# Performance work log

Hardware: AMD Instinct MI355X
Metric: run time of the kernel (lower is better)

## Reference

```python
import jax, jax.numpy as jnp
import numpy as np

B, N, F_IN, F_OUT, H = 8, 1024, 64, 128, 4
D = F_OUT // H  # head_dim = 32
NEG_SLOPE = 0.2


def setup_inputs() -> dict:
    key = jax.random.key(0)
    k1, k2, k3, k4, k5 = jax.random.split(key, 5)
    x = jax.random.normal(k1, (B, N, F_IN), dtype=jnp.float32)
    adj = jax.random.randint(k2, (N, N), 0, 2, dtype=jnp.int32)
    edge_weights = jax.random.uniform(k3, (N, N), dtype=jnp.float32)
    W = jax.random.normal(k4, (F_IN, F_OUT), dtype=jnp.float32) * (1.0 / np.sqrt(F_IN))
    a = jax.random.normal(k5, (H, 2 * D), dtype=jnp.float32) * (1.0 / np.sqrt(2 * D))
    return {"x": x, "adj": adj, "edge_weights": edge_weights, "W": W, "a": a}


def reference(x, adj, edge_weights, W, a):
    # x: [B,N,F_in], adj: [N,N] int, edge_weights: [N,N], W: [F_in,F_out], a: [H,2D]
    b, n, _ = x.shape
    h = (x @ W).reshape(b, n, H, D)  # [B,N,H,D]
    # e[b,i,j,h] = leaky_relu(a_src . h_i + a_dst . h_j)  (equivalent to concat trick)
    e_src = jnp.einsum('bnhd,hd->bnh', h, a[:, :D])  # [B,N,H]
    e_dst = jnp.einsum('bnhd,hd->bnh', h, a[:, D:])  # [B,N,H]
    e = jax.nn.leaky_relu(e_src[:, :, None, :] + e_dst[:, None, :, :], NEG_SLOPE)  # [B,N,N,H]
    mask = (adj == 0)[None, :, :, None]  # [1,N,N,1]
    e = jnp.where(mask, -jnp.inf, e)
    # numerically-stable softmax over neighbors (axis=2), matching torch reference
    e_max = jnp.max(e, axis=2, keepdims=True)
    e_max = jnp.where(jnp.isinf(e_max), 0.0, e_max)
    e_stable = e - e_max
    e_stable = jnp.where(jnp.isinf(e_stable), -100.0, e_stable)
    attn = jax.nn.softmax(e_stable, axis=2)
    attn = jnp.where(jnp.isnan(attn), 0.0, attn)
    # dropout is identity in eval mode
    attn = attn * edge_weights[None, :, :, None]  # [B,N,N,H]
    out = jnp.einsum('bijh,bjhd->bihd', attn, h).reshape(b, n, H * D)  # [B,N,F_out]
    avg_attn = attn.mean(axis=-1)  # [B,N,N]
    return out, avg_attn
```

## Files before the change

### kernel.cpp

```cpp
#include <hip/hip_runtime.h>
#include <hip/hip_bf16.h>

constexpr int B  = 8;
constexpr int N  = 1024;
constexpr int FI = 64;
constexpr int FO = 128;
constexpr int NH = 4;
constexpr float LOG2E = 1.4426950408889634f;

using short8 = __attribute__((ext_vector_type(8))) short;
using f32x4  = __attribute__((ext_vector_type(4))) float;

union I8 { int4 v[2]; int s[8]; };
union F8 { float4 v[2]; float s[8]; };

__device__ __forceinline__ unsigned bfpack(float a, float b) {
  __hip_bfloat162 r = __float22bfloat162_rn(make_float2(a, b));
  union { __hip_bfloat162 h; unsigned u; } c; c.h = r; return c.u;
}
__device__ __forceinline__ float bf2f(unsigned short u) {
  union { unsigned int b; float f; } c; c.b = (unsigned int)u << 16; return c.f;
}

__global__ __launch_bounds__(256) void gat_mask(
    const int* __restrict__ adj, const float* __restrict__ ew,
    unsigned short* __restrict__ mew) {
  const size_t base = ((size_t)blockIdx.x * 256 + threadIdx.x) * 8;
  I8 aj; aj.v[0] = *(const int4*)(adj + base); aj.v[1] = *(const int4*)(adj + base + 4);
  F8 e;  e.v[0]  = *(const float4*)(ew + base); e.v[1]  = *(const float4*)(ew + base + 4);
  union { unsigned short u[8]; uint4 v; } o;
  #pragma unroll
  for (int u = 0; u < 8; ++u) {
    __hip_bfloat16 hb = __float2bfloat16(e.s[u]);
    unsigned short bits = *reinterpret_cast<unsigned short*>(&hb);
    o.u[u] = aj.s[u] ? bits : (unsigned short)0x8000;
  }
  *(uint4*)(mew + base) = o.v;
}

__global__ __launch_bounds__(256, 2) void gat_proj(
    const float* __restrict__ x, const float* __restrict__ W,
    const float* __restrict__ a,
    unsigned short* __restrict__ h_hi, unsigned short* __restrict__ h_lo,
    float* __restrict__ es, float* __restrict__ edt) {
  __shared__ float xs[16 * FI];
  const int t = threadIdx.x;
  const int row0 = blockIdx.x * 16;
  for (int i = t; i < 16 * FI; i += 256) xs[i] = x[row0 * FI + i];
  const int f  = t & 127;
  const int rh = t >> 7;
  float wc[FI];
  #pragma unroll
  for (int k = 0; k < FI; ++k) wc[k] = W[k * FO + f];
  const int hh = f >> 5, d = f & 31;
  const float a_s = a[hh * 64 + d] * LOG2E;
  const float a_d = a[hh * 64 + 32 + d] * LOG2E;
  __syncthreads();
  float acc8[8];
  #pragma unroll
  for (int r = 0; r < 8; ++r) {
    const int lr = rh * 8 + r;
    const float4* xr = (const float4*)(xs + lr * FI);
    float acc = 0.f;
    #pragma unroll
    for (int kq = 0; kq < FI / 4; ++kq) {
      const float4 xv = xr[kq];
      acc += xv.x * wc[4*kq] + xv.y * wc[4*kq+1] + xv.z * wc[4*kq+2] + xv.w * wc[4*kq+3];
    }
    acc8[r] = acc;
    float ps = acc * a_s, pd = acc * a_d;
    #pragma unroll
    for (int off = 16; off; off >>= 1) {
      ps += __shfl_xor(ps, off, 64);
      pd += __shfl_xor(pd, off, 64);
    }
    const int row = row0 + lr;
    if (d == 0) {
      es[row * NH + hh] = ps;
      edt[((size_t)((row >> 10) * NH + hh)) * N + (row & 1023)] = pd;
    }
  }
  const int bb = row0 >> 10;
  const int jl = (row0 & 1023) + rh * 8;
  union { unsigned short u16[8]; uint4 v; } hi, lo;
  #pragma unroll
  for (int r = 0; r < 8; ++r) {
    __hip_bfloat16 hb = __float2bfloat16(acc8[r]);
    hi.u16[r] = *reinterpret_cast<unsigned short*>(&hb);
    float res = acc8[r] - __bfloat162float(hb);
    __hip_bfloat16 lb = __float2bfloat16(res);
    lo.u16[r] = *reinterpret_cast<unsigned short*>(&lb);
  }
  const int ft = f >> 4, n = f & 15;
  const int sS = jl >> 5, kq2 = (jl >> 3) & 3;
  const size_t base = (size_t)bb * (FO * N)
                    + ((size_t)(ft * 32 + sS) * 64 + (n + 16 * kq2)) * 8;
  *(uint4*)(h_hi + base) = hi.v;
  *(uint4*)(h_lo + base) = lo.v;
}

__global__ __launch_bounds__(512, 2) void gat_attn(
    const unsigned short* __restrict__ h_hi, const unsigned short* __restrict__ h_lo,
    const float* __restrict__ es, const float* __restrict__ edt,
    const unsigned short* __restrict__ mew,
    float* __restrict__ out, float* __restrict__ dinv) {
  __shared__ unsigned short pew[2][4 * 2048];
  __shared__ float dvl[64];
  const int t  = threadIdx.x;
  const int b  = blockIdx.x & 7;
  const int i0 = (blockIdx.x >> 3) << 4;
  const int il = t >> 5, jq = t & 31;
  const int gi = i0 + il;
  float esv[4];
  { const float4 e4 = *(const float4*)(es + ((size_t)b * N + gi) * NH);
    esv[0] = e4.x; esv[1] = e4.y; esv[2] = e4.z; esv[3] = e4.w; }
  const int lane = t & 63, wave = t >> 6;
  const int hh = wave & 3, nt2 = wave >> 2;
  const int m = lane & 15, kq = lane >> 4;
  const int ft = hh * 2 + nt2;
  const unsigned short* hb_hi = h_hi + (size_t)b * (FO * N) + (size_t)(ft * 32) * 512 + lane * 8;
  const unsigned short* hb_lo = h_lo + (size_t)b * (FO * N) + (size_t)(ft * 32) * 512 + lane * 8;
  f32x4 acc0 = {0.f,0.f,0.f,0.f}, acc1 = {0.f,0.f,0.f,0.f};
  f32x4 acc2 = {0.f,0.f,0.f,0.f}, acc3 = {0.f,0.f,0.f,0.f};
  float dpart[4] = {0.f, 0.f, 0.f, 0.f};

  auto p1_step = [&](int c, int buf) {
    const int jb = c * 128 + jq * 4;
    union { unsigned v2[2]; unsigned short u[4]; } mw;
    *(uint2*)mw.v2 = *(const uint2*)(mew + (size_t)gi * N + jb);
    float edh[4][4];
    #pragma unroll
    for (int h = 0; h < 4; ++h) {
      const float4 e4 = *(const float4*)(edt + ((size_t)(b * NH + h)) * N + jb);
      edh[h][0] = e4.x; edh[h][1] = e4.y; edh[h][2] = e4.z; edh[h][3] = e4.w;
    }
    float pw[4][4];
    #pragma unroll
    for (int u = 0; u < 4; ++u) {
      const float mfa = bf2f((unsigned short)(mw.u[u] & 0x7fff));
      const float sgn = (mw.u[u] >> 15) ? 0.f : 1.f;
      #pragma unroll
      for (int h = 0; h < 4; ++h) {
        float e = esv[h] + edh[h][u];
        e = fmaxf(e, 0.2f * e);
        const float p = __builtin_amdgcn_exp2f(e);
        pw[h][u] = p * mfa;
        dpart[h] = fmaf(p, sgn, dpart[h]);
      }
    }
    const int g = jq >> 1, half = jq & 1;
    const int o = ((g * 16 + il) ^ (g & 7)) * 8 + half * 4;
    #pragma unroll
    for (int h = 0; h < 4; ++h) {
      uint2 pk = { bfpack(pw[h][0], pw[h][1]), bfpack(pw[h][2], pw[h][3]) };
      *(uint2*)(pew[buf] + h * 2048 + o) = pk;
    }
  };

  short8 Bh[4], Bl[4];
  #pragma unroll
  for (int ks = 0; ks < 4; ++ks) {
    Bh[ks] = *(const short8*)(hb_hi + (size_t)ks * 512);
    Bl[ks] = *(const short8*)(hb_lo + (size_t)ks * 512);
  }
  p1_step(0, 0);
  __syncthreads();

  for (int c = 0; c < 8; ++c) {
    short8 Ph[4], Pl[4];
    if (c + 1 < 8) {
      p1_step(c + 1, (c + 1) & 1);
      const size_t so = (size_t)(c + 1) * 4 * 512;
      #pragma unroll
      for (int ks = 0; ks < 4; ++ks) {
        Ph[ks] = *(const short8*)(hb_hi + so + (size_t)ks * 512);
        Pl[ks] = *(const short8*)(hb_lo + so + (size_t)ks * 512);
      }
    }
    {
      const int buf = c & 1;
      #pragma unroll
      for (int ks = 0; ks < 4; ++ks) {
        const int g2 = ks * 4 + kq;
        const int o2 = ((g2 * 16 + m) ^ (g2 & 7)) * 8;
        short8 afr;
        { uint4 tmp = *(const uint4*)(pew[buf] + hh * 2048 + o2);
          __builtin_memcpy(&afr, &tmp, 16); }
        if (ks & 1) {
          acc2 = __builtin_amdgcn_mfma_f32_16x16x32_bf16(afr, Bh[ks], acc2, 0, 0, 0);
          acc3 = __builtin_amdgcn_mfma_f32_16x16x32_bf16(afr, Bl[ks], acc3, 0, 0, 0);
        } else {
          acc0 = __builtin_amdgcn_mfma_f32_16x16x32_bf16(afr, Bh[ks], acc0, 0, 0, 0);
          acc1 = __builtin_amdgcn_mfma_f32_16x16x32_bf16(afr, Bl[ks], acc1, 0, 0, 0);
        }
      }
    }
    if (c + 1 < 8) __syncthreads();
    #pragma unroll
    for (int ks = 0; ks < 4; ++ks) { Bh[ks] = Ph[ks]; Bl[ks] = Pl[ks]; }
  }

  #pragma unroll
  for (int h = 0; h < 4; ++h) {
    float v = dpart[h];
    v += __shfl_xor(v, 1, 64);  v += __shfl_xor(v, 2, 64);
    v += __shfl_xor(v, 4, 64);  v += __shfl_xor(v, 8, 64);
    v += __shfl_xor(v, 16, 64);
    if (jq == 0) dvl[il * NH + h] = v;
  }
  __syncthreads();
  if (t < 64) { const float dd = dvl[t]; dvl[t] = dd > 0.f ? 1.0f / dd : 0.f; }
  __syncthreads();
  if (t < 64) dinv[((size_t)b * N + i0) * NH + t] = dvl[t];
  #pragma unroll
  for (int reg = 0; reg < 4; ++reg) {
    const int row = kq * 4 + reg;
    const float inv = dvl[row * NH + hh];
    out[((size_t)b * N + i0 + row) * FO + hh * 32 + nt2 * 16 + m]
        = (acc0[reg] + acc1[reg] + acc2[reg] + acc3[reg]) * inv;
  }
}

__global__ __launch_bounds__(256, 4) void gat_avg(
    const float* __restrict__ es, const float* __restrict__ edt,
    const unsigned short* __restrict__ mew, const float* __restrict__ dinv,
    float* __restrict__ avg) {
  const int t  = threadIdx.x;
  const int b  = blockIdx.x & 7;
  const int i0 = (blockIdx.x >> 3) << 2;
  const int il = t >> 6, jq = t & 63;
  const int gi = i0 + il;
  float esv[4], inv4[4];
  { const float4 e4 = *(const float4*)(es + ((size_t)b * N + gi) * NH);
    esv[0] = e4.x; esv[1] = e4.y; esv[2] = e4.z; esv[3] = e4.w; }
  { const float4 d4 = *(const float4*)(dinv + ((size_t)b * N + gi) * NH);
    inv4[0] = d4.x; inv4[1] = d4.y; inv4[2] = d4.z; inv4[3] = d4.w; }
  #pragma unroll
  for (int c = 0; c < 4; ++c) {
    const int jb = c * 256 + jq * 4;
    union { uint2 v; unsigned short u[4]; } mw;
    mw.v = *(const uint2*)(mew + (size_t)gi * N + jb);
    float edh[4][4];
    #pragma unroll
    for (int h = 0; h < 4; ++h) {
      const float4 e4 = *(const float4*)(edt + ((size_t)(b * NH + h)) * N + jb);
      edh[h][0] = e4.x; edh[h][1] = e4.y; edh[h][2] = e4.z; edh[h][3] = e4.w;
    }
    float4 r;
    float* rp = &r.x;
    #pragma unroll
    for (int u = 0; u < 4; ++u) {
      const float mfa = bf2f((unsigned short)(mw.u[u] & 0x7fff));
      float sv = 0.f;
      #pragma unroll
      for (int h = 0; h < 4; ++h) {
        float e = esv[h] + edh[h][u];
        e = fmaxf(e, 0.2f * e);
        sv += __builtin_amdgcn_exp2f(e) * inv4[h];
      }
      rp[u] = 0.25f * mfa * sv;
    }
    *(float4*)(avg + ((size_t)b * N + gi) * N + jb) = r;
  }
}

extern "C" void kernel_launch(void* const* d_in, const int* in_sizes, int n_in,
                              void* d_out, int out_size, void* d_ws, size_t ws_size,
                              hipStream_t stream) {
  const float* x   = (const float*)d_in[0];
  const int*   adj = (const int*)d_in[1];
  const float* ewt = (const float*)d_in[2];
  const float* W   = (const float*)d_in[3];
  const float* a   = (const float*)d_in[4];

  float* out = (float*)d_out;
  float* avg = out + (size_t)B * N * FO;

  unsigned short* hhi = (unsigned short*)d_ws;
  unsigned short* hlo = hhi + (size_t)B * FO * N;
  unsigned short* mew = hlo + (size_t)B * FO * N;
  float* es   = (float*)(mew + (size_t)N * N);
  float* edt  = es + (size_t)B * N * NH;
  float* dnv  = edt + (size_t)B * NH * N;

  gat_mask<<<(N * N) / 2048, 256, 0, stream>>>(adj, ewt, mew);
  gat_proj<<<(B * N) / 16, 256, 0, stream>>>(x, W, a, hhi, hlo, es, edt);
  gat_attn<<<B * (N / 16), 512, 0, stream>>>(hhi, hlo, es, edt, mew, out, dnv);
  gat_avg<<<B * (N / 4), 256, 0, stream>>>(es, edt, mew, dnv, avg);
}
```

Baseline: 115.4 us.

## Fuse mask/proj kernels and fold avg-attention pass into attention kernel

The mask-building and projection kernels are merged into one launch, with blocks split by index. The separate avg-attention kernel is removed: each attention block writes its own avg_attn rows right after computing the softmax denominators, so the dinv round trip and two launches go away. The main loop is also restructured to issue next-chunk loads earlier. Occupancy is raised to 4 blocks per CU, which may add register pressure or spills.

Result: faster. 110.0 us (-4.7%).

```diff
diff --git a/kernel.cpp b/kernel.cpp
--- a/kernel.cpp
+++ b/kernel.cpp
@@ -22,29 +22,29 @@
   union { unsigned int b; float f; } c; c.b = (unsigned int)u << 16; return c.f;
 }
 
-__global__ __launch_bounds__(256) void gat_mask(
-    const int* __restrict__ adj, const float* __restrict__ ew,
+__global__ __launch_bounds__(256, 2) void gat_prep(
+    const float* __restrict__ x, const float* __restrict__ W,
+    const float* __restrict__ a, const int* __restrict__ adj,
+    const float* __restrict__ ew,
+    unsigned short* __restrict__ h_hi, unsigned short* __restrict__ h_lo,
+    float* __restrict__ es, float* __restrict__ edt,
     unsigned short* __restrict__ mew) {
-  const size_t base = ((size_t)blockIdx.x * 256 + threadIdx.x) * 8;
-  I8 aj; aj.v[0] = *(const int4*)(adj + base); aj.v[1] = *(const int4*)(adj + base + 4);
-  F8 e;  e.v[0]  = *(const float4*)(ew + base); e.v[1]  = *(const float4*)(ew + base + 4);
-  union { unsigned short u[8]; uint4 v; } o;
-  #pragma unroll
-  for (int u = 0; u < 8; ++u) {
-    __hip_bfloat16 hb = __float2bfloat16(e.s[u]);
-    unsigned short bits = *reinterpret_cast<unsigned short*>(&hb);
-    o.u[u] = aj.s[u] ? bits : (unsigned short)0x8000;
-  }
-  *(uint4*)(mew + base) = o.v;
-}
-
-__global__ __launch_bounds__(256, 2) void gat_proj(
-    const float* __restrict__ x, const float* __restrict__ W,
-    const float* __restrict__ a,
-    unsigned short* __restrict__ h_hi, unsigned short* __restrict__ h_lo,
-    float* __restrict__ es, float* __restrict__ edt) {
+  const int t = threadIdx.x;
+  if (blockIdx.x >= 512) {
+    const size_t base = ((size_t)(blockIdx.x - 512) * 256 + t) * 8;
+    I8 aj; aj.v[0] = *(const int4*)(adj + base); aj.v[1] = *(const int4*)(adj + base + 4);
+    F8 e;  e.v[0]  = *(const float4*)(ew + base); e.v[1]  = *(const float4*)(ew + base + 4);
+    union { unsigned short u[8]; uint4 v; } o;
+    #pragma unroll
+    for (int u = 0; u < 8; ++u) {
+      __hip_bfloat16 hb = __float2bfloat16(e.s[u]);
+      unsigned short bits = *reinterpret_cast<unsigned short*>(&hb);
+      o.u[u] = aj.s[u] ? bits : (unsigned short)0x8000;
+    }
+    *(uint4*)(mew + base) = o.v;
+    return;
+  }
   __shared__ float xs[16 * FI];
-  const int t = threadIdx.x;
   const int row0 = blockIdx.x * 16;
   for (int i = t; i < 16 * FI; i += 256) xs[i] = x[row0 * FI + i];
   const int f  = t & 127;
@@ -99,11 +99,11 @@
   *(uint4*)(h_lo + base) = lo.v;
 }
 
-__global__ __launch_bounds__(512, 2) void gat_attn(
+__global__ __launch_bounds__(512, 4) void gat_attn(
     const unsigned short* __restrict__ h_hi, const unsigned short* __restrict__ h_lo,
     const float* __restrict__ es, const float* __restrict__ edt,
     const unsigned short* __restrict__ mew,
-    float* __restrict__ out, float* __restrict__ dinv) {
+    float* __restrict__ out, float* __restrict__ avg) {
   __shared__ unsigned short pew[2][4 * 2048];
   __shared__ float dvl[64];
   const int t  = threadIdx.x;
@@ -124,80 +124,88 @@
   f32x4 acc2 = {0.f,0.f,0.f,0.f}, acc3 = {0.f,0.f,0.f,0.f};
   float dpart[4] = {0.f, 0.f, 0.f, 0.f};
 
-  auto p1_step = [&](int c, int buf) {
+  uint2  rmw;
+  float4 red[4];
+  short8 Bh[4], Bl[4];
+
+  auto ld_p1 = [&](int c) {
     const int jb = c * 128 + jq * 4;
-    union { unsigned v2[2]; unsigned short u[4]; } mw;
-    *(uint2*)mw.v2 = *(const uint2*)(mew + (size_t)gi * N + jb);
-    float edh[4][4];
-    #pragma unroll
-    for (int h = 0; h < 4; ++h) {
-      const float4 e4 = *(const float4*)(edt + ((size_t)(b * NH + h)) * N + jb);
-      edh[h][0] = e4.x; edh[h][1] = e4.y; edh[h][2] = e4.z; edh[h][3] = e4.w;
-    }
-    float pw[4][4];
-    #pragma unroll
-    for (int u = 0; u < 4; ++u) {
-      const float mfa = bf2f((unsigned short)(mw.u[u] & 0x7fff));
-      const float sgn = (mw.u[u] >> 15) ? 0.f : 1.f;
-      #pragma unroll
-      for (int h = 0; h < 4; ++h) {
-        float e = esv[h] + edh[h][u];
-        e = fmaxf(e, 0.2f * e);
-        const float p = __builtin_amdgcn_exp2f(e);
-        pw[h][u] = p * mfa;
-        dpart[h] = fmaf(p, sgn, dpart[h]);
-      }
-    }
+    rmw = *(const uint2*)(mew + (size_t)gi * N + jb);
+    #pragma unroll
+    for (int h = 0; h < 4; ++h)
+      red[h] = *(const float4*)(edt + ((size_t)(b * NH + h)) * N + jb);
+  };
+  auto ld_B = [&](int c) {
+    const size_t so = (size_t)c * 4 * 512;
+    #pragma unroll
+    for (int ks = 0; ks < 4; ++ks) {
+      Bh[ks] = *(const short8*)(hb_hi + so + (size_t)ks * 512);
+      Bl[ks] = *(const short8*)(hb_lo + so + (size_t)ks * 512);
+    }
+  };
+  auto p1_compute = [&](int c) {
+    const int buf = c & 1;
+    union { uint2 v; unsigned short u[4]; } mw; mw.v = rmw;
     const int g = jq >> 1, half = jq & 1;
     const int o = ((g * 16 + il) ^ (g & 7)) * 8 + half * 4;
     #pragma unroll
-    for (int h = 0; h < 4; ++h) {
-      uint2 pk = { bfpack(pw[h][0], pw[h][1]), bfpack(pw[h][2], pw[h][3]) };
-      *(uint2*)(pew[buf] + h * 2048 + o) = pk;
-    }
-  };
-
-  short8 Bh[4], Bl[4];
-  #pragma unroll
-  for (int ks = 0; ks < 4; ++ks) {
-    Bh[ks] = *(const short8*)(hb_hi + (size_t)ks * 512);
-    Bl[ks] = *(const short8*)(hb_lo + (size_t)ks * 512);
-  }
-  p1_step(0, 0);
-  __syncthreads();
-
+    for (int up = 0; up < 2; ++up) {
+      float pk[4][2];
+      #pragma unroll
+      for (int uu = 0; uu < 2; ++uu) {
+        const int u = up * 2 + uu;
+        const float mfa = bf2f((unsigned short)(mw.u[u] & 0x7fff));
+        const float sgn = (mw.u[u] >> 15) ? 0.f : 1.f;
+        const float* ep = &red[0].x;
+        #pragma unroll
+        for (int h = 0; h < 4; ++h) {
+          float e = esv[h] + (&red[h].x)[u];
+          e = fmaxf(e, 0.2f * e);
+          const float p = __builtin_amdgcn_exp2f(e);
+          pk[h][uu] = p * mfa;
+          dpart[h] = fmaf(p, sgn, dpart[h]);
+        }
+        (void)ep;
+      }
+      #pragma unroll
+      for (int h = 0; h < 4; ++h)
+        *(unsigned*)(pew[buf] + h * 2048 + o + up * 2) = bfpack(pk[h][0], pk[h][1]);
+    }
+  };
+  auto p2_step = [&](int c) {
+    const int buf = c & 1;
+    #pragma unroll
+    for (int ks = 0; ks < 4; ++ks) {
+      const int g2 = ks * 4 + kq;
+      const int o2 = ((g2 * 16 + m) ^ (g2 & 7)) * 8;
+      short8 afr;
+      { uint4 tmp = *(const uint4*)(pew[buf] + hh * 2048 + o2);
+        __builtin_memcpy(&afr, &tmp, 16); }
+      if (ks & 1) {
+        acc2 = __builtin_amdgcn_mfma_f32_16x16x32_bf16(afr, Bh[ks], acc2, 0, 0, 0);
+        acc3 = __builtin_amdgcn_mfma_f32_16x16x32_bf16(afr, Bl[ks], acc3, 0, 0, 0);
+      } else {
+        acc0 = __builtin_amdgcn_mfma_f32_16x16x32_bf16(afr, Bh[ks], acc0, 0, 0, 0);
+        acc1 = __builtin_amdgcn_mfma_f32_16x16x32_bf16(afr, Bl[ks], acc1, 0, 0, 0);
+      }
+    }
+  };
+
+  ld_B(0);
+  ld_p1(0);
+  p1_compute(0);
+  ld_p1(1);
+  __syncthreads();
+
+  #pragma unroll 1
   for (int c = 0; c < 8; ++c) {
-    short8 Ph[4], Pl[4];
+    p2_step(c);
     if (c + 1 < 8) {
-      p1_step(c + 1, (c + 1) & 1);
-      const size_t so = (size_t)(c + 1) * 4 * 512;
-      #pragma unroll
-      for (int ks = 0; ks < 4; ++ks) {
-        Ph[ks] = *(const short8*)(hb_hi + so + (size_t)ks * 512);
-        Pl[ks] = *(const short8*)(hb_lo + so + (size_t)ks * 512);
-      }
-    }
-    {
-      const int buf = c & 1;
-      #pragma unroll
-      for (int ks = 0; ks < 4; ++ks) {
-        const int g2 = ks * 4 + kq;
-        const int o2 = ((g2 * 16 + m) ^ (g2 & 7)) * 8;
-        short8 afr;
-        { uint4 tmp = *(const uint4*)(pew[buf] + hh * 2048 + o2);
-          __builtin_memcpy(&afr, &tmp, 16); }
-        if (ks & 1) {
-          acc2 = __builtin_amdgcn_mfma_f32_16x16x32_bf16(afr, Bh[ks], acc2, 0, 0, 0);
-          acc3 = __builtin_amdgcn_mfma_f32_16x16x32_bf16(afr, Bl[ks], acc3, 0, 0, 0);
-        } else {
-          acc0 = __builtin_amdgcn_mfma_f32_16x16x32_bf16(afr, Bh[ks], acc0, 0, 0, 0);
-          acc1 = __builtin_amdgcn_mfma_f32_16x16x32_bf16(afr, Bl[ks], acc1, 0, 0, 0);
-        }
-      }
-    }
-    if (c + 1 < 8) __syncthreads();
-    #pragma unroll
-    for (int ks = 0; ks < 4; ++ks) { Bh[ks] = Ph[ks]; Bl[ks] = Pl[ks]; }
+      ld_B(c + 1);
+      p1_compute(c + 1);
+      if (c + 2 < 8) ld_p1(c + 2);
+      __syncthreads();
+    }
   }
 
   #pragma unroll
@@ -211,7 +219,6 @@
   __syncthreads();
   if (t < 64) { const float dd = dvl[t]; dvl[t] = dd > 0.f ? 1.0f / dd : 0.f; }
   __syncthreads();
-  if (t < 64) dinv[((size_t)b * N + i0) * NH + t] = dvl[t];
   #pragma unroll
   for (int reg = 0; reg < 4; ++reg) {
     const int row = kq * 4 + reg;
@@ -219,33 +226,18 @@
     out[((size_t)b * N + i0 + row) * FO + hh * 32 + nt2 * 16 + m]
         = (acc0[reg] + acc1[reg] + acc2[reg] + acc3[reg]) * inv;
   }
-}
-
-__global__ __launch_bounds__(256, 4) void gat_avg(
-    const float* __restrict__ es, const float* __restrict__ edt,
-    const unsigned short* __restrict__ mew, const float* __restrict__ dinv,
-    float* __restrict__ avg) {
-  const int t  = threadIdx.x;
-  const int b  = blockIdx.x & 7;
-  const int i0 = (blockIdx.x >> 3) << 2;
-  const int il = t >> 6, jq = t & 63;
-  const int gi = i0 + il;
-  float esv[4], inv4[4];
-  { const float4 e4 = *(const float4*)(es + ((size_t)b * N + gi) * NH);
-    esv[0] = e4.x; esv[1] = e4.y; esv[2] = e4.z; esv[3] = e4.w; }
-  { const float4 d4 = *(const float4*)(dinv + ((size_t)b * N + gi) * NH);
-    inv4[0] = d4.x; inv4[1] = d4.y; inv4[2] = d4.z; inv4[3] = d4.w; }
-  #pragma unroll
-  for (int c = 0; c < 4; ++c) {
-    const int jb = c * 256 + jq * 4;
+  float inv4[4];
+  #pragma unroll
+  for (int h = 0; h < 4; ++h) inv4[h] = dvl[il * NH + h];
+  #pragma unroll 1
+  for (int c = 0; c < 8; ++c) {
+    const int jb = c * 128 + jq * 4;
     union { uint2 v; unsigned short u[4]; } mw;
     mw.v = *(const uint2*)(mew + (size_t)gi * N + jb);
-    float edh[4][4];
-    #pragma unroll
-    for (int h = 0; h < 4; ++h) {
-      const float4 e4 = *(const float4*)(edt + ((size_t)(b * NH + h)) * N + jb);
-      edh[h][0] = e4.x; edh[h][1] = e4.y; edh[h][2] = e4.z; edh[h][3] = e4.w;
-    }
+    float4 ed4[4];
+    #pragma unroll
+    for (int h = 0; h < 4; ++h)
+      ed4[h] = *(const float4*)(edt + ((size_t)(b * NH + h)) * N + jb);
     float4 r;
     float* rp = &r.x;
     #pragma unroll
@@ -254,7 +246,7 @@
       float sv = 0.f;
       #pragma unroll
       for (int h = 0; h < 4; ++h) {
-        float e = esv[h] + edh[h][u];
+        float e = esv[h] + (&ed4[h].x)[u];
         e = fmaxf(e, 0.2f * e);
         sv += __builtin_amdgcn_exp2f(e) * inv4[h];
       }
@@ -281,10 +273,7 @@
   unsigned short* mew = hlo + (size_t)B * FO * N;
   float* es   = (float*)(mew + (size_t)N * N);
   float* edt  = es + (size_t)B * N * NH;
-  float* dnv  = edt + (size_t)B * NH * N;
-
-  gat_mask<<<(N * N) / 2048, 256, 0, stream>>>(adj, ewt, mew);
-  gat_proj<<<(B * N) / 16, 256, 0, stream>>>(x, W, a, hhi, hlo, es, edt);
-  gat_attn<<<B * (N / 16), 512, 0, stream>>>(hhi, hlo, es, edt, mew, out, dnv);
-  gat_avg<<<B * (N / 4), 256, 0, stream>>>(es, edt, mew, dnv, avg);
-}
+
+  gat_prep<<<1024, 256, 0, stream>>>(x, W, a, adj, ewt, hhi, hlo, es, edt, mew);
+  gat_attn<<<B * (N / 16), 512, 0, stream>>>(hhi, hlo, es, edt, mew, out, avg);
+}
```
